# Kernel tuning notes

Hardware: AMD Instinct MI355X
Metric: run time of the kernel (lower is better)

## Reference

```python
import jax, jax.numpy as jnp
import numpy as np

B, S, HID = 4, 2048, 2048
H, HKV, D = 16, 4, 128
RANK = 512
SCALE = D ** -0.5


def setup_inputs() -> dict:
    key = jax.random.key(0)
    ks = jax.random.split(key, 5)
    scale_w = 0.02
    return {
        "hidden_states": jax.random.normal(ks[0], (B, S, HID), dtype=jnp.float32),
        "Wq": jax.random.normal(ks[1], (HID, H * D), dtype=jnp.float32) * scale_w,
        "Wc": jax.random.normal(ks[2], (HID, RANK), dtype=jnp.float32) * scale_w,
        "Wup": jax.random.normal(ks[3], (RANK, HKV * D), dtype=jnp.float32) * scale_w,
        "Wo": jax.random.normal(ks[4], (H * D, HID), dtype=jnp.float32) * scale_w,
    }


def reference(hidden_states, Wq, Wc, Wup, Wo):
    b, s, _ = hidden_states.shape
    n_rep = H // HKV
    # Q projection -> (b, H, s, D)
    q = (hidden_states @ Wq).reshape(b, s, H, D).transpose(0, 2, 1, 3)
    # low-rank KV compression -> (b, s, RANK)
    kv_c = hidden_states @ Wc
    # gate in source is ones -> sigmoid(1) constant scalar multiply
    kv_c = kv_c * jax.nn.sigmoid(jnp.float32(1.0))
    # decompress: single kv_up_proj produces shared K/V content
    kv = (kv_c @ Wup).reshape(b, s, HKV, D).transpose(0, 2, 1, 3)  # (b, HKV, s, D)
    k = jnp.repeat(kv, n_rep, axis=1)  # (b, H, s, D), repeat_interleave over heads
    v = k
    scores = jnp.einsum("bhqd,bhkd->bhqk", q, k) * SCALE
    attn = jax.nn.softmax(scores.astype(jnp.float32), axis=-1).astype(q.dtype)
    out = jnp.einsum("bhqk,bhkd->bhqd", attn, v)
    out = out.transpose(0, 2, 1, 3).reshape(b, s, H * D)
    return out @ Wo
```

## Files before the change

### kernel.cpp

```cpp
#include <hip/hip_runtime.h>
#include <hip/hip_bf16.h>
#include <stdint.h>

#define DEV __device__ __forceinline__

typedef __bf16 bf16x8 __attribute__((ext_vector_type(8)));
typedef float f32x4 __attribute__((ext_vector_type(4)));
typedef float f32x16 __attribute__((ext_vector_type(16)));
typedef int i32x4 __attribute__((ext_vector_type(4)));


DEV void gload_lds16(const void* g, void* l) {
  __builtin_amdgcn_global_load_lds((const __attribute__((address_space(1))) void*)g,
                                   (__attribute__((address_space(3))) void*)l, 16, 0, 0);
}

__global__ __launch_bounds__(256) void k_cast(const float* __restrict__ in,
                                              __hip_bfloat16* __restrict__ out, int n) {
  int i = (blockIdx.x * 256 + threadIdx.x) * 8;
  if (i >= n) return;
  const float4* p = (const float4*)(in + i);
  float4 a = p[0], c = p[1];
  bf16x8 v;
  v[0] = (__bf16)a.x; v[1] = (__bf16)a.y; v[2] = (__bf16)a.z; v[3] = (__bf16)a.w;
  v[4] = (__bf16)c.x; v[5] = (__bf16)c.y; v[6] = (__bf16)c.z; v[7] = (__bf16)c.w;
  *(bf16x8*)(out + i) = v;
}

__global__ __launch_bounds__(256) void k_tcast(const float* __restrict__ in,
                                               __hip_bfloat16* __restrict__ out, int R, int C) {
  __shared__ float t[32][33];
  int c0 = blockIdx.x * 32, r0 = blockIdx.y * 32;
  int x = threadIdx.x, y0 = threadIdx.y;
  for (int j = y0; j < 32; j += 8) t[j][x] = in[(size_t)(r0 + j) * C + c0 + x];
  __syncthreads();
  for (int j = y0; j < 32; j += 8)
    out[(size_t)(c0 + j) * R + r0 + x] = __float2bfloat16(t[x][j]);
}

__global__ __launch_bounds__(256) void k_tbf16(const __hip_bfloat16* __restrict__ in,
                                               __hip_bfloat16* __restrict__ out) {
  __shared__ unsigned short t[32][33];
  int z = blockIdx.z;
  const unsigned short* ip = (const unsigned short*)in + (size_t)z * 2048 * 128;
  unsigned short* op = (unsigned short*)out + (size_t)z * 2048 * 128;
  int d0 = blockIdx.x * 32, s0 = blockIdx.y * 32;
  int x = threadIdx.x, y0 = threadIdx.y;
  for (int j = y0; j < 32; j += 8) t[j][x] = ip[(size_t)(s0 + j) * 128 + d0 + x];
  __syncthreads();
  for (int j = y0; j < 32; j += 8) op[(size_t)(d0 + j) * 2048 + s0 + x] = t[x][j];
}

template <int MODE>
__global__ __launch_bounds__(256, 2) void k_gemm(const __hip_bfloat16* __restrict__ A,
                                                 const __hip_bfloat16* __restrict__ BT,
                                                 void* __restrict__ Cout,
                                                 int M, int N, int K, float scale) {
  __shared__ __align__(16) __hip_bfloat16 As[128 * 64];
  __shared__ __align__(16) __hip_bfloat16 Bs[128 * 64];
  const int tid = threadIdx.x;
  const int lane = tid & 63, wid = tid >> 6;
  const int g = lane >> 4, lr = lane & 15;
  const int m0 = blockIdx.x * 128, n0 = blockIdx.y * 128;
  const int wr = wid >> 1, wc = wid & 1;
  const f32x4 vzero = {0.f, 0.f, 0.f, 0.f};

  f32x4 acc[4][4];
#pragma unroll
  for (int i = 0; i < 4; ++i)
#pragma unroll
    for (int j = 0; j < 4; ++j) acc[i][j] = vzero;

  const char* aSrc[4];
  const char* bSrc[4];
  char* aDst[4];
  char* bDst[4];
#pragma unroll
  for (int i = 0; i < 4; ++i) {
    int p = i * 4096 + tid * 16;
    int row = p >> 7, colb = p & 127;
    int scol = colb ^ ((row & 7) << 4);
    aSrc[i] = (const char*)A + ((size_t)(m0 + row) * K) * 2 + scol;
    bSrc[i] = (const char*)BT + ((size_t)(n0 + row) * K) * 2 + scol;
    aDst[i] = (char*)As + i * 4096 + wid * 1024;
    bDst[i] = (char*)Bs + i * 4096 + wid * 1024;
  }

  const int nk = K >> 6;
  for (int kt = 0; kt < nk; ++kt) {
    const size_t ko = (size_t)kt * 128;
#pragma unroll
    for (int i = 0; i < 4; ++i) gload_lds16(aSrc[i] + ko, aDst[i]);
#pragma unroll
    for (int i = 0; i < 4; ++i) gload_lds16(bSrc[i] + ko, bDst[i]);
    __syncthreads();
#pragma unroll
    for (int kc = 0; kc < 2; ++kc) {
      bf16x8 af[4], bfr[4];
#pragma unroll
      for (int fm = 0; fm < 4; ++fm) {
        int row = wr * 64 + fm * 16 + lr;
        int cb = (kc * 64 + g * 16) ^ ((row & 7) << 4);
        af[fm] = *(const bf16x8*)((const char*)As + row * 128 + cb);
      }
#pragma unroll
      for (int fn = 0; fn < 4; ++fn) {
        int row = wc * 64 + fn * 16 + lr;
        int cb = (kc * 64 + g * 16) ^ ((row & 7) << 4);
        bfr[fn] = *(const bf16x8*)((const char*)Bs + row * 128 + cb);
      }
#pragma unroll
      for (int fm = 0; fm < 4; ++fm)
#pragma unroll
        for (int fn = 0; fn < 4; ++fn)
          acc[fm][fn] =
              __builtin_amdgcn_mfma_f32_16x16x32_bf16(af[fm], bfr[fn], acc[fm][fn], 0, 0, 0);
    }
    __syncthreads();
  }

#pragma unroll
  for (int fm = 0; fm < 4; ++fm) {
#pragma unroll
    for (int fn = 0; fn < 4; ++fn) {
      const int mb = m0 + wr * 64 + fm * 16 + g * 4;
      const int n = n0 + wc * 64 + fn * 16 + lr;
#pragma unroll
      for (int r = 0; r < 4; ++r) {
        float v = acc[fm][fn][r] * scale;
        int m = mb + r;
        if constexpr (MODE == 2) {
          int b = m >> 11, s = m & 2047, hk = n >> 7, d = n & 127;
          ((__hip_bfloat16*)Cout)[(((size_t)(b * 4 + hk) * 2048) + s) * 128 + d] =
              __float2bfloat16(v);
        } else {
          ((__hip_bfloat16*)Cout)[(size_t)n * M + m] = __float2bfloat16(v);
        }
      }
    }
  }
}

template <int MODE>
__global__ __launch_bounds__(512, 2) void k_gemm256(const __hip_bfloat16* __restrict__ A,
                                                    const __hip_bfloat16* __restrict__ BT,
                                                    void* __restrict__ Cout,
                                                    int M, int N, int K, float scale) {
  __shared__ __align__(16) char smem[131072];
  const int tid = threadIdx.x;
  const int lane = tid & 63, wid = tid >> 6;
  const int lr = lane & 15, g = lane >> 4;
  const int bid = blockIdx.x;
  const int swz = (bid & 7) * 32 + (bid >> 3);
  const int m0 = (swz & 31) * 256, n0 = (swz >> 5) * 256;
  const int wr = wid >> 2, wc = wid & 3;
  const size_t K2 = (size_t)K * 2;
  const f32x4 vzero = {0.f, 0.f, 0.f, 0.f};

  const int srow = tid >> 3, sslot = tid & 7;
  const int sw = (sslot ^ (srow & 7)) << 4;
  const char* gA = (const char*)A + (size_t)(m0 + srow) * K2 + sw;
  const char* gB = (const char*)BT + (size_t)(n0 + srow) * K2 + sw;
  const size_t hG = (size_t)128 * K2;
  const size_t r2 = (size_t)64 * K2;
  char* const ldsW = smem + wid * 1024;

  auto stageH = [&](int isB, int half, int buf, size_t ko) {
    const char* src = (isB ? gB : gA) + (half ? hG : 0) + ko;
    char* dst = ldsW + buf * 65536 + isB * 32768 + half * 16384;
    gload_lds16(src, dst);
    gload_lds16(src + r2, dst + 8192);
  };

  const int rowA = (wr * 64 + lr) * 128;
  const int rowB = (wc * 32 + lr) * 128;
  const int sl0 = ((0 ^ (lr & 7)) << 4);
  bf16x8 a[8], b0[4], b1[4];
  auto ldA = [&](int buf, int mh) {
    const char* p = smem + buf * 65536 + mh * 16384 + rowA;
#pragma unroll
    for (int rb = 0; rb < 4; ++rb)
#pragma unroll
      for (int kc = 0; kc < 2; ++kc)
        a[rb * 2 + kc] =
            *(const bf16x8*)(p + rb * 2048 + (((kc * 4 + g) ^ (lr & 7)) << 4));
  };
  auto ldB = [&](int buf, int nh, bf16x8 (&b)[4]) {
    const char* p = smem + buf * 65536 + 32768 + nh * 16384 + rowB;
#pragma unroll
    for (int rb = 0; rb < 2; ++rb)
#pragma unroll
      for (int kc = 0; kc < 2; ++kc)
        b[rb * 2 + kc] =
            *(const bf16x8*)(p + rb * 2048 + (((kc * 4 + g) ^ (lr & 7)) << 4));
  };

  f32x4 acc[8][4];
#pragma unroll
  for (int i = 0; i < 8; ++i)
#pragma unroll
    for (int j = 0; j < 4; ++j) acc[i][j] = vzero;

  auto mm = [&](bf16x8 (&b)[4], int fmB, int fnB) {
    __builtin_amdgcn_s_setprio(1);
#pragma unroll
    for (int kc = 0; kc < 2; ++kc)
#pragma unroll
      for (int rb = 0; rb < 4; ++rb)
#pragma unroll
        for (int nb = 0; nb < 2; ++nb)
          acc[fmB + rb][fnB + nb] = __builtin_amdgcn_mfma_f32_16x16x32_bf16(
              a[rb * 2 + kc], b[nb * 2 + kc], acc[fmB + rb][fnB + nb], 0, 0, 0);
    __builtin_amdgcn_s_setprio(0);
  };

  auto tile = [&](int buf, size_t ko1, size_t ko2, bool s1, bool s2, bool w6, bool w0) {
    ldA(buf, 0);
    ldB(buf, 0, b0);
    if (s1) stageH(0, 1, buf ^ 1, ko1);
    asm volatile("s_waitcnt lgkmcnt(8)" ::: "memory");
    __builtin_amdgcn_s_barrier();
    asm volatile("s_waitcnt lgkmcnt(0)" ::: "memory");
    __builtin_amdgcn_sched_barrier(0);
    mm(b0, 0, 0);
    __builtin_amdgcn_s_barrier();
    ldB(buf, 1, b1);
    if (s2) stageH(0, 0, buf, ko2);
    __builtin_amdgcn_s_barrier();
    asm volatile("s_waitcnt lgkmcnt(0)" ::: "memory");
    __builtin_amdgcn_sched_barrier(0);
    mm(b1, 0, 2);
    __builtin_amdgcn_s_barrier();
    ldA(buf, 1);
    if (s2) stageH(1, 0, buf, ko2);
    __builtin_amdgcn_s_barrier();
    asm volatile("s_waitcnt lgkmcnt(0)" ::: "memory");
    __builtin_amdgcn_sched_barrier(0);
    mm(b1, 4, 2);
    __builtin_amdgcn_s_barrier();
    if (s2) stageH(1, 1, buf, ko2);
    __builtin_amdgcn_s_barrier();
    __builtin_amdgcn_sched_barrier(0);
    mm(b0, 4, 0);
    if (w6) asm volatile("s_waitcnt vmcnt(6)" ::: "memory");
    else if (w0) asm volatile("s_waitcnt vmcnt(0)" ::: "memory");
    __builtin_amdgcn_s_barrier();
  };

  stageH(0, 0, 0, 0);
  stageH(1, 0, 0, 0);
  stageH(1, 1, 0, 0);
  stageH(0, 1, 0, 0);
  stageH(0, 0, 1, 128);
  stageH(1, 0, 1, 128);
  stageH(1, 1, 1, 128);
  asm volatile("s_waitcnt vmcnt(6)" ::: "memory");
  __builtin_amdgcn_s_barrier();

  const int nk = K >> 6;
#pragma unroll 1
  for (int t = 0; t < nk - 2; t += 2) {
    tile(0, (size_t)(t + 1) * 128, (size_t)(t + 2) * 128, true, true, true, false);
    tile(1, (size_t)(t + 2) * 128, (size_t)(t + 3) * 128, true, true, true, false);
  }
  tile(0, (size_t)(nk - 1) * 128, 0, true, false, false, true);
  tile(1, 0, 0, false, false, false, false);

#pragma unroll
  for (int fm = 0; fm < 8; ++fm) {
    const int mrow = m0 + (fm >> 2) * 128 + wr * 64 + (fm & 3) * 16 + g * 4;
#pragma unroll
    for (int fn = 0; fn < 4; ++fn) {
      const int n = n0 + (fn >> 1) * 128 + wc * 32 + (fn & 1) * 16 + lr;
#pragma unroll
      for (int r = 0; r < 4; ++r) {
        float v = acc[fm][fn][r] * scale;
        int m = mrow + r;
        if constexpr (MODE == 0) {
          ((float*)Cout)[(size_t)m * N + n] = v;
        } else {
          int b = m >> 11, s = m & 2047, h = n >> 7, d = n & 127;
          ((__hip_bfloat16*)Cout)[(((size_t)(b * 16 + h) * 2048) + s) * 128 + d] =
              __float2bfloat16(v);
        }
      }
    }
  }
}

__global__ __launch_bounds__(512, 2) void k_attn2(const __hip_bfloat16* __restrict__ q,
                                                  const __hip_bfloat16* __restrict__ kv,
                                                  const __hip_bfloat16* __restrict__ kvT,
                                                  __hip_bfloat16* __restrict__ out) {
  __shared__ __align__(16) char smem[65536];
  const int tid = threadIdx.x, lane = tid & 63, wid = tid >> 6;
  const int hi = lane >> 5, lq = lane & 31;
  const int qt = blockIdx.x;
  const int pair = blockIdx.y;
  const int b = pair >> 2, hkv = pair & 3;
  const int h = hkv * 4 + (wid & 3);
  const int q0w = qt * 64 + (wid >> 2) * 32;

  const char* qrow =
      (const char*)q + (((size_t)(b * 16 + h) * 2048 + q0w + lq) * 128 + hi * 8) * 2;
  bf16x8 qfr[8];
#pragma unroll
  for (int kt = 0; kt < 8; ++kt) qfr[kt] = *(const bf16x8*)(qrow + kt * 32);

  const char* kbase = (const char*)kv + ((size_t)pair * 2048 * 128) * 2;
  const char* tbase = (const char*)kvT + ((size_t)pair * 2048 * 128) * 2;
  const char* pK;
  const char* pV;
  {
    int p0 = tid * 16;
    int krow = p0 >> 8, kcol = p0 & 255;
    pK = kbase + (size_t)krow * 256 + (kcol ^ ((krow & 15) << 4));
    int vrow = p0 >> 7, vcol = p0 & 127;
    pV = tbase + (size_t)vrow * 4096 + (vcol ^ ((vrow & 7) << 4));
  }

  f32x16 accO[4];
#pragma unroll
  for (int dt = 0; dt < 4; ++dt)
#pragma unroll
    for (int i = 0; i < 16; ++i) accO[dt][i] = 0.f;
  float m_run = -1e30f, l_run = 0.f;

  const int hsK = (hi * 16) ^ ((lq & 15) << 4);
  const int hsV = (hi * 16) ^ ((lq & 7) << 4);

  auto stage = [&](int kb, int vb) {
    gload_lds16(pK, smem + kb + wid * 1024);
    gload_lds16(pK + 8192, smem + kb + 8192 + wid * 1024);
    gload_lds16(pV, smem + vb + wid * 1024);
    gload_lds16(pV + 262144, smem + vb + 8192 + wid * 1024);
    pK += 16384;
    pV += 128;
  };

  auto compute = [&](int kb, int vb) {
    f32x16 st[2];
#pragma unroll
    for (int i = 0; i < 16; ++i) { st[0][i] = 0.f; st[1][i] = 0.f; }
    const char* Kb = smem + kb;
#pragma unroll
    for (int tau = 0; tau < 2; ++tau) {
      const char* Kr = Kb + (tau * 32 + lq) * 256;
#pragma unroll
      for (int kt = 0; kt < 8; ++kt) {
        bf16x8 kf = *(const bf16x8*)(Kr + ((kt * 32) ^ hsK));
        st[tau] = __builtin_amdgcn_mfma_f32_32x32x16_bf16(kf, qfr[kt], st[tau], 0, 0, 0);
      }
    }
    float mloc[8];
#pragma unroll
    for (int i = 0; i < 8; ++i)
      mloc[i] = fmaxf(fmaxf(st[0][i], st[0][i + 8]), fmaxf(st[1][i], st[1][i + 8]));
#pragma unroll
    for (int i = 0; i < 4; ++i) mloc[i] = fmaxf(mloc[i], mloc[i + 4]);
    float pm = fmaxf(fmaxf(mloc[0], mloc[1]), fmaxf(mloc[2], mloc[3]));
    pm = fmaxf(pm, __shfl_xor(pm, 32));
    if (__any(pm > m_run + 8.f)) {
      float mnew = fmaxf(m_run, pm);
      float alpha = __builtin_amdgcn_exp2f(m_run - mnew);
      m_run = mnew;
      l_run *= alpha;
#pragma unroll
      for (int dt = 0; dt < 4; ++dt)
#pragma unroll
        for (int i = 0; i < 16; ++i) accO[dt][i] *= alpha;
    }
    float p0[16], p1[16];
#pragma unroll
    for (int i = 0; i < 16; ++i) p0[i] = __builtin_amdgcn_exp2f(st[0][i] - m_run);
#pragma unroll
    for (int i = 0; i < 16; ++i) p1[i] = __builtin_amdgcn_exp2f(st[1][i] - m_run);
    float s0 = 0.f, s1 = 0.f, s2 = 0.f, s3 = 0.f;
#pragma unroll
    for (int i = 0; i < 8; ++i) {
      s0 += p0[i]; s1 += p0[i + 8]; s2 += p1[i]; s3 += p1[i + 8];
    }
    l_run += (s0 + s1) + (s2 + s3);
    bf16x8 pfr[4];
#pragma unroll
    for (int ks = 0; ks < 4; ++ks) {
      const int base = (ks & 1) * 8;
      int A0, A1, B0, B1;
      if (ks < 2) {
        asm("v_cvt_pk_bf16_f32 %0, %1, %2" : "=v"(A0) : "v"(p0[base + 0]), "v"(p0[base + 1]));
        asm("v_cvt_pk_bf16_f32 %0, %1, %2" : "=v"(A1) : "v"(p0[base + 2]), "v"(p0[base + 3]));
        asm("v_cvt_pk_bf16_f32 %0, %1, %2" : "=v"(B0) : "v"(p0[base + 4]), "v"(p0[base + 5]));
        asm("v_cvt_pk_bf16_f32 %0, %1, %2" : "=v"(B1) : "v"(p0[base + 6]), "v"(p0[base + 7]));
      } else {
        asm("v_cvt_pk_bf16_f32 %0, %1, %2" : "=v"(A0) : "v"(p1[base + 0]), "v"(p1[base + 1]));
        asm("v_cvt_pk_bf16_f32 %0, %1, %2" : "=v"(A1) : "v"(p1[base + 2]), "v"(p1[base + 3]));
        asm("v_cvt_pk_bf16_f32 %0, %1, %2" : "=v"(B0) : "v"(p1[base + 4]), "v"(p1[base + 5]));
        asm("v_cvt_pk_bf16_f32 %0, %1, %2" : "=v"(B1) : "v"(p1[base + 6]), "v"(p1[base + 7]));
      }
      asm("v_permlane32_swap_b32 %0, %1" : "+v"(A0), "+v"(B0));
      asm("v_permlane32_swap_b32 %0, %1" : "+v"(A1), "+v"(B1));
      union { int w[4]; bf16x8 v; } u;
      u.w[0] = A0; u.w[1] = A1; u.w[2] = B0; u.w[3] = B1;
      pfr[ks] = u.v;
    }
    const char* Vb = smem + vb;
#pragma unroll
    for (int dt = 0; dt < 4; ++dt) {
      const char* Vr = Vb + (dt * 32 + lq) * 128;
#pragma unroll
      for (int ks = 0; ks < 4; ++ks) {
        bf16x8 vf = *(const bf16x8*)(Vr + ((ks * 32) ^ hsV));
        accO[dt] = __builtin_amdgcn_mfma_f32_32x32x16_bf16(vf, pfr[ks], accO[dt], 0, 0, 0);
      }
    }
  };

  stage(0, 32768);
  __syncthreads();
#pragma unroll 1
  for (int it = 0; it < 16; ++it) {
    stage(16384, 49152);
    compute(0, 32768);
    __syncthreads();
    if (it < 15) stage(0, 32768);
    compute(16384, 49152);
    __syncthreads();
  }

  float lt = l_run + __shfl_xor(l_run, 32);
  float inv = 1.f / lt;
#pragma unroll
  for (int dt = 0; dt < 4; ++dt)
#pragma unroll
    for (int i = 0; i < 16; ++i) accO[dt][i] *= inv;

  __syncthreads();
  char* scr = smem + wid * 8192;
  const int swq = (lq & 15) << 4;
#pragma unroll
  for (int dt = 0; dt < 4; ++dt) {
#pragma unroll
    for (int rp = 0; rp < 8; ++rp) {
      int w;
      asm("v_cvt_pk_bf16_f32 %0, %1, %2"
          : "=v"(w)
          : "v"(accO[dt][2 * rp]), "v"(accO[dt][2 * rp + 1]));
      int dloc = ((2 * rp) & 3) + 8 * (rp >> 1) + 4 * hi;
      int bytec = (dt * 64 + dloc * 2) ^ swq;
      *(int*)(scr + lq * 256 + bytec) = w;
    }
  }
  __syncthreads();
  const int l16 = lane & 15, lh = lane >> 4;
#pragma unroll
  for (int ps = 0; ps < 8; ++ps) {
    int qr = ps * 4 + lh;
    i32x4 v = *(const i32x4*)(scr + qr * 256 + ((l16 * 16) ^ ((qr & 15) << 4)));
    char* dst = (char*)out + (((size_t)(b * 2048 + q0w + qr) * 2048) + h * 128 + l16 * 8) * 2;
    *(i32x4*)dst = v;
  }
}

extern "C" void kernel_launch(void* const* d_in, const int* in_sizes, int n_in,
                              void* d_out, int out_size, void* d_ws, size_t ws_size,
                              hipStream_t stream) {
  const float* hs = (const float*)d_in[0];
  const float* Wq = (const float*)d_in[1];
  const float* Wc = (const float*)d_in[2];
  const float* Wup = (const float*)d_in[3];
  const float* Wo = (const float*)d_in[4];

  if (ws_size < 105381888u) return;
  char* ws = (char*)d_ws;
  __hip_bfloat16* hs_bf = (__hip_bfloat16*)(ws + 0);
  __hip_bfloat16* q_attn = (__hip_bfloat16*)(ws + 33554432);
  __hip_bfloat16* kvb = (__hip_bfloat16*)(ws + 67108864);
  __hip_bfloat16* kvT = (__hip_bfloat16*)(ws + 75497472);
  __hip_bfloat16* WqT = (__hip_bfloat16*)(ws + 83886080);
  __hip_bfloat16* WoT = (__hip_bfloat16*)(ws + 92274688);
  __hip_bfloat16* WupT = (__hip_bfloat16*)(ws + 100663296);
  __hip_bfloat16* Wc_bf = (__hip_bfloat16*)(ws + 101187584);
  __hip_bfloat16* WckvT = (__hip_bfloat16*)(ws + 103284736);
  __hip_bfloat16* attnout = hs_bf;

  const float qscale = (float)(0.08838834764831845 * 1.4426950408889634);

  k_cast<<<8192, 256, 0, stream>>>(hs, hs_bf, 16777216);
  k_cast<<<512, 256, 0, stream>>>(Wc, Wc_bf, 1048576);
  k_tcast<<<dim3(64, 64), dim3(32, 8), 0, stream>>>(Wq, WqT, 2048, 2048);
  k_tcast<<<dim3(64, 64), dim3(32, 8), 0, stream>>>(Wo, WoT, 2048, 2048);
  k_tcast<<<dim3(16, 16), dim3(32, 8), 0, stream>>>(Wup, WupT, 512, 512);
  k_gemm<3><<<dim3(16, 4), 256, 0, stream>>>(Wc_bf, WupT, WckvT, 2048, 512, 512,
                                             0.7310585786300049f);
  k_gemm256<1><<<256, 512, 0, stream>>>(hs_bf, WqT, q_attn, 8192, 2048, 2048, qscale);
  k_gemm<2><<<dim3(64, 4), 256, 0, stream>>>(hs_bf, WckvT, kvb, 8192, 512, 2048, 1.0f);
  k_tbf16<<<dim3(4, 64, 16), dim3(32, 8), 0, stream>>>(kvb, kvT);
  k_attn2<<<dim3(32, 16), 512, 0, stream>>>(q_attn, kvb, kvT, attnout);
  k_gemm256<0><<<256, 512, 0, stream>>>(attnout, WoT, d_out, 8192, 2048, 2048, 1.0f);
}
```

Measured before the change: 348.4 us.

## Software-pipeline attention loop: overlap QK^T of next tile with softmax/PV of current

Splits the attention tile compute into a QK^T phase and a softmax+PV phase, then skews them so the next tile's score MFMAs are issued alongside the previous tile's softmax and PV work. V buffers grow to a 4-deep ring, raising LDS to 96KB, and __syncthreads is replaced by explicit vmcnt waits plus raw barriers. The goal is to hide softmax latency and memory waits behind MFMA work, at the cost of more registers (two score accumulators) and more LDS, which may lower occupancy under launch_bounds(512,2).

```diff
diff --git a/kernel.cpp b/kernel.cpp
--- a/kernel.cpp
+++ b/kernel.cpp
@@ -174,7 +174,6 @@
 
   const int rowA = (wr * 64 + lr) * 128;
   const int rowB = (wc * 32 + lr) * 128;
-  const int sl0 = ((0 ^ (lr & 7)) << 4);
   bf16x8 a[8], b0[4], b1[4];
   auto ldA = [&](int buf, int mh) {
     const char* p = smem + buf * 65536 + mh * 16384 + rowA;
@@ -292,7 +291,7 @@
                                                   const __hip_bfloat16* __restrict__ kv,
                                                   const __hip_bfloat16* __restrict__ kvT,
                                                   __hip_bfloat16* __restrict__ out) {
-  __shared__ __align__(16) char smem[65536];
+  __shared__ __align__(16) char smem[98304];
   const int tid = threadIdx.x, lane = tid & 63, wid = tid >> 6;
   const int hi = lane >> 5, lq = lane & 31;
   const int qt = blockIdx.x;
@@ -338,8 +337,7 @@
     pV += 128;
   };
 
-  auto compute = [&](int kb, int vb) {
-    f32x16 st[2];
+  auto qkt = [&](f32x16 (&st)[2], int kb) {
 #pragma unroll
     for (int i = 0; i < 16; ++i) { st[0][i] = 0.f; st[1][i] = 0.f; }
     const char* Kb = smem + kb;
@@ -352,6 +350,9 @@
         st[tau] = __builtin_amdgcn_mfma_f32_32x32x16_bf16(kf, qfr[kt], st[tau], 0, 0, 0);
       }
     }
+  };
+
+  auto finish = [&](f32x16 (&st)[2], int vb) {
     float mloc[8];
 #pragma unroll
     for (int i = 0; i < 8; ++i)
@@ -415,17 +416,35 @@
     }
   };
 
+  f32x16 stA[2], stB[2];
+
   stage(0, 32768);
+  asm volatile("s_waitcnt vmcnt(0)" ::: "memory");
   __syncthreads();
+  stage(16384, 32768 + 16384);
+  qkt(stA, 0);
+  asm volatile("s_waitcnt vmcnt(2)" ::: "memory");
+  __builtin_amdgcn_s_barrier();
 #pragma unroll 1
-  for (int it = 0; it < 16; ++it) {
-    stage(16384, 49152);
-    compute(0, 32768);
-    __syncthreads();
-    if (it < 15) stage(0, 32768);
-    compute(16384, 49152);
-    __syncthreads();
-  }
+  for (int it = 0; it < 15; ++it) {
+    const int t1 = 2 * it + 1;
+    stage(0, 32768 + (((t1 + 1) & 3) << 14));
+    qkt(stB, 16384);
+    finish(stA, 32768 + (((t1 - 1) & 3) << 14));
+    asm volatile("s_waitcnt vmcnt(2)" ::: "memory");
+    __builtin_amdgcn_s_barrier();
+    const int t2 = 2 * it + 2;
+    stage(16384, 32768 + (((t2 + 1) & 3) << 14));
+    qkt(stA, 0);
+    finish(stB, 32768 + (((t2 - 1) & 3) << 14));
+    asm volatile("s_waitcnt vmcnt(2)" ::: "memory");
+    __builtin_amdgcn_s_barrier();
+  }
+  qkt(stB, 16384);
+  finish(stA, 32768 + (2 << 14));
+  asm volatile("s_waitcnt vmcnt(0)" ::: "memory");
+  __builtin_amdgcn_s_barrier();
+  finish(stB, 32768 + (3 << 14));
 
   float lt = l_run + __shfl_xor(l_run, 32);
   float inv = 1.f / lt;
```

New measurement: 356.7 us. +2.4%, slower.
